# Performance work log

Measured on AMD Instinct MI355X. Metric: run time of the kernel, lower is better.

Reference implementation:

```python
import jax, jax.numpy as jnp
import numpy as np

N_NODES = 50000
N_EDGES = 1_000_000
N_HYPER = 1024
F_IN = 128
F_EDGE = 64


def setup_inputs() -> dict:
    key = jax.random.key(0)
    ks = jax.random.split(key, 20)
    s = 0.05
    return {
        "x": jax.random.normal(ks[0], (N_NODES, F_IN), jnp.float32),
        "edge_index": jax.random.randint(ks[1], (2, N_EDGES), 0, N_NODES, dtype=jnp.int64),
        "edge_weight": jax.random.uniform(ks[2], (N_EDGES,), jnp.float32),
        "edge_features": jax.random.normal(ks[3], (N_HYPER, F_EDGE), jnp.float32),
        "adj_e": jax.random.uniform(ks[4], (N_HYPER, N_HYPER), jnp.float32) / N_HYPER,
        "T": jax.random.uniform(ks[5], (N_NODES, N_HYPER), jnp.float32) / N_HYPER,
        # HypergraphConvLayer 1: 128 -> 64
        "W1": jax.random.normal(ks[6], (F_IN, 64), jnp.float32) * s,
        "b1": jnp.zeros((64,), jnp.float32),
        # HypergraphConvLayer 2: 64 -> 32
        "W2": jax.random.normal(ks[7], (64, 32), jnp.float32) * s,
        "b2": jnp.zeros((32,), jnp.float32),
        # GraphConvolution (CensNet-style): node 32->32, edge 64->32
        "Wn": jax.random.normal(ks[8], (32, 32), jnp.float32) * s,
        "We": jax.random.normal(ks[9], (F_EDGE, 32), jnp.float32) * s,
        "bg": jnp.zeros((32,), jnp.float32),
        # class_classifier: Linear(32,32) -> ReLU -> Linear(32,2) -> Softmax
        "Wc1": jax.random.normal(ks[10], (32, 32), jnp.float32) * s,
        "bc1": jnp.zeros((32,), jnp.float32),
        "Wc2": jax.random.normal(ks[11], (32, 2), jnp.float32) * s,
        "bc2": jnp.zeros((2,), jnp.float32),
    }


def _hconv(h, W, b, src, dst, edge_weight, num_nodes):
    # linear projection then edge-weighted scatter-add: out[dst] += w * h[src]
    h = h @ W + b
    msg = h[src] * edge_weight[:, None]          # [E, d]
    return jax.ops.segment_sum(msg, dst, num_segments=num_nodes)


def reference(x, edge_index, edge_weight, edge_features, adj_e, T,
              W1, b1, W2, b2, Wn, We, bg, Wc1, bc1, Wc2, bc2):
    n = x.shape[0]
    src, dst = edge_index[0], edge_index[1]

    h = jax.nn.relu(_hconv(x, W1, b1, src, dst, edge_weight, n))   # [N,64]
    h = jax.nn.relu(_hconv(h, W2, b2, src, dst, edge_weight, n))   # [N,32]

    # aggregate_node_features: node_features[dst] += h[src]; / num_edges
    num_edges = edge_index.shape[1]
    node_features = jax.ops.segment_sum(h[src], dst, num_segments=n) / num_edges

    # edge_conv: node linear + incidence-weighted hyperedge convolution
    edge_h = adj_e @ (edge_features @ We)                           # [NE,32]
    shared = jax.nn.relu(node_features @ Wn + T @ edge_h + bg)      # [N,32]

    # class_classifier
    c = jax.nn.relu(shared @ Wc1 + bc1)
    logits = c @ Wc2 + bc2
    return jax.nn.softmax(logits, axis=1)                           # [N,2]
```

## Files before the change

kernel.cpp:

```cpp
#include <hip/hip_runtime.h>
#include <hip/hip_bf16.h>

#define RPB 256

template<int COLS, int K>
__global__ __launch_bounds__(256) void gemm_k(
    const float* __restrict__ X, const float* __restrict__ W,
    const float* __restrict__ bias, float* __restrict__ out,
    int nrows, float scale, int relu_in)
{
    constexpr int CPT = COLS / 8;
    constexpr int KT  = 32;
    constexpr int NKT = K / KT;

    __shared__ float sx[RPB * 36];
    __shared__ float sWT[COLS * 33];

    const int tid = threadIdx.x;
    const int cg  = tid & 7;
    const int rg  = tid >> 3;
    const int r0  = blockIdx.x * RPB;

    float acc[8][CPT];
    #pragma unroll
    for (int r = 0; r < 8; ++r)
        #pragma unroll
        for (int c = 0; c < CPT; ++c) acc[r][c] = 0.f;

    for (int kt = 0; kt < NKT; ++kt) {
        #pragma unroll
        for (int j = 0; j < 8; ++j) {
            int i  = tid + j * 256;
            int r  = i >> 3;
            int k4 = i & 7;
            int gr = r0 + r; if (gr >= nrows) gr = nrows - 1;
            float4 v = *(const float4*)&X[(size_t)gr * K + kt * KT + k4 * 4];
            if (relu_in) {
                v.x = fmaxf(v.x, 0.f); v.y = fmaxf(v.y, 0.f);
                v.z = fmaxf(v.z, 0.f); v.w = fmaxf(v.w, 0.f);
            }
            if (scale != 1.f) { v.x *= scale; v.y *= scale; v.z *= scale; v.w *= scale; }
            *(float4*)&sx[r * 36 + k4 * 4] = v;
        }
        for (int i = tid; i < COLS * KT; i += 256) {
            int kl = i / COLS, c = i % COLS;
            sWT[c * 33 + kl] = W[(size_t)(kt * KT + kl) * COLS + c];
        }
        __syncthreads();

        #pragma unroll
        for (int k4 = 0; k4 < 8; ++k4) {
            float4 a[8];
            #pragma unroll
            for (int r = 0; r < 8; ++r)
                a[r] = *(const float4*)&sx[(r * 32 + rg) * 36 + k4 * 4];
            #pragma unroll
            for (int cc = 0; cc < CPT; ++cc) {
                int c = cg * CPT + cc;
                float w0 = sWT[c * 33 + k4 * 4 + 0];
                float w1 = sWT[c * 33 + k4 * 4 + 1];
                float w2 = sWT[c * 33 + k4 * 4 + 2];
                float w3 = sWT[c * 33 + k4 * 4 + 3];
                #pragma unroll
                for (int r = 0; r < 8; ++r)
                    acc[r][cc] += a[r].x * w0 + a[r].y * w1 + a[r].z * w2 + a[r].w * w3;
            }
        }
        __syncthreads();
    }

    #pragma unroll
    for (int r = 0; r < 8; ++r) {
        int row = r0 + r * 32 + rg;
        if (row < nrows) {
            #pragma unroll
            for (int cc4 = 0; cc4 < CPT / 4; ++cc4) {
                int c = cg * CPT + cc4 * 4;
                float4 o;
                o.x = acc[r][cc4 * 4 + 0] + (bias ? bias[c + 0] : 0.f);
                o.y = acc[r][cc4 * 4 + 1] + (bias ? bias[c + 1] : 0.f);
                o.z = acc[r][cc4 * 4 + 2] + (bias ? bias[c + 2] : 0.f);
                o.w = acc[r][cc4 * 4 + 3] + (bias ? bias[c + 3] : 0.f);
                *(float4*)&out[(size_t)row * COLS + c] = o;
            }
        }
    }
}

__global__ __launch_bounds__(256, 4) void tgemm2_k(
    const float* __restrict__ T, const float* __restrict__ eh,
    float* __restrict__ par, int nrows)
{
    __shared__ float seh[256 * 32];
    const int tid = threadIdx.x;
    const int ks  = blockIdx.y * 256;

    #pragma unroll
    for (int j = 0; j < 8; ++j) {
        int i = tid + j * 256;
        *(float4*)&seh[i * 4] = *(const float4*)&eh[(size_t)ks * 32 + (size_t)i * 4];
    }
    __syncthreads();

    int row = blockIdx.x * 256 + tid;
    int r   = row < nrows ? row : nrows - 1;
    const float* Tp = T + (size_t)r * 1024 + ks;

    float acc[32];
    #pragma unroll
    for (int c = 0; c < 32; ++c) acc[c] = 0.f;

    float4 t[8];
    #pragma unroll
    for (int q = 0; q < 8; ++q) t[q] = *(const float4*)&Tp[q * 4];

    for (int kc = 0; kc < 8; ++kc) {
        float4 tn[8];
        if (kc < 7) {
            #pragma unroll
            for (int q = 0; q < 8; ++q)
                tn[q] = *(const float4*)&Tp[(kc + 1) * 32 + q * 4];
        }
        #pragma unroll
        for (int q = 0; q < 8; ++q) {
            #pragma unroll
            for (int j = 0; j < 4; ++j) {
                float a = (j == 0) ? t[q].x : (j == 1) ? t[q].y : (j == 2) ? t[q].z : t[q].w;
                int k = kc * 32 + q * 4 + j;
                #pragma unroll
                for (int c4 = 0; c4 < 8; ++c4) {
                    float4 w = *(const float4*)&seh[k * 32 + c4 * 4];
                    acc[c4 * 4 + 0] += a * w.x;
                    acc[c4 * 4 + 1] += a * w.y;
                    acc[c4 * 4 + 2] += a * w.z;
                    acc[c4 * 4 + 3] += a * w.w;
                }
            }
        }
        #pragma unroll
        for (int q = 0; q < 8; ++q) t[q] = tn[q];
    }

    if (row < nrows) {
        float* p = par + (size_t)blockIdx.y * nrows * 32 + (size_t)row * 32;
        #pragma unroll
        for (int c4 = 0; c4 < 8; ++c4)
            *(float4*)&p[c4 * 4] = make_float4(acc[c4 * 4 + 0], acc[c4 * 4 + 1],
                                               acc[c4 * 4 + 2], acc[c4 * 4 + 3]);
    }
}

__global__ __launch_bounds__(256) void classify_k(
    const float* __restrict__ par, const float* __restrict__ nfw,
    const float* __restrict__ bg, const float* __restrict__ Wc1,
    const float* __restrict__ bc1, const float* __restrict__ Wc2,
    const float* __restrict__ bc2, float* __restrict__ out, int nrows)
{
    __shared__ float sWc1T[1024];
    __shared__ float sWc2[64];
    __shared__ float sb[66];

    int tid = threadIdx.x;
    for (int i = tid; i < 1024; i += 256)
        sWc1T[(i & 31) * 32 + (i >> 5)] = Wc1[i];
    if (tid < 64) sWc2[tid] = Wc2[tid];
    if (tid < 32)      sb[tid] = bc1[tid];
    else if (tid < 64) sb[tid] = bg[tid - 32];
    else if (tid < 66) sb[tid] = bc2[tid - 64];
    __syncthreads();

    int row = blockIdx.x * 256 + tid;
    if (row >= nrows) return;

    size_t stride = (size_t)nrows * 32;
    float4 sh4[8];
    #pragma unroll
    for (int i4 = 0; i4 < 8; ++i4) {
        const float* base = par + (size_t)row * 32 + i4 * 4;
        float4 v0 = *(const float4*)(base);
        float4 v1 = *(const float4*)(base + stride);
        float4 v2 = *(const float4*)(base + 2 * stride);
        float4 v3 = *(const float4*)(base + 3 * stride);
        float4 nf = *(const float4*)&nfw[(size_t)row * 32 + i4 * 4];
        float4 o;
        o.x = fmaxf(v0.x + v1.x + v2.x + v3.x + nf.x + sb[32 + i4 * 4 + 0], 0.f);
        o.y = fmaxf(v0.y + v1.y + v2.y + v3.y + nf.y + sb[32 + i4 * 4 + 1], 0.f);
        o.z = fmaxf(v0.z + v1.z + v2.z + v3.z + nf.z + sb[32 + i4 * 4 + 2], 0.f);
        o.w = fmaxf(v0.w + v1.w + v2.w + v3.w + nf.w + sb[32 + i4 * 4 + 3], 0.f);
        sh4[i4] = o;
    }

    float l0 = sb[64], l1 = sb[65];
    #pragma unroll
    for (int jj = 0; jj < 32; ++jj) {
        float s = sb[jj];
        #pragma unroll
        for (int i4 = 0; i4 < 8; ++i4) {
            float4 w4 = *(const float4*)&sWc1T[jj * 32 + i4 * 4];
            s += sh4[i4].x * w4.x + sh4[i4].y * w4.y
               + sh4[i4].z * w4.z + sh4[i4].w * w4.w;
        }
        s = fmaxf(s, 0.f);
        l0 += s * sWc2[jj * 2 + 0];
        l1 += s * sWc2[jj * 2 + 1];
    }
    float p0 = 1.f / (1.f + expf(l1 - l0));
    float p1 = 1.f / (1.f + expf(l0 - l1));
    *(float2*)&out[(size_t)row * 2] = make_float2(p0, p1);
}

__global__ void hist_k(const int* __restrict__ dst, int* __restrict__ deg, int E)
{
    int e = blockIdx.x * 256 + threadIdx.x;
    if (e < E) atomicAdd(&deg[dst[e]], 1);
}

__global__ void scan1_k(const int* __restrict__ deg, int* __restrict__ bsum, int N)
{
    __shared__ int s[256];
    int t = threadIdx.x, i = blockIdx.x * 256 + t;
    s[t] = (i < N) ? deg[i] : 0;
    __syncthreads();
    for (int off = 128; off > 0; off >>= 1) {
        if (t < off) s[t] += s[t + off];
        __syncthreads();
    }
    if (t == 0) bsum[blockIdx.x] = s[0];
}

__global__ void scan2_k(const int* __restrict__ bsum, int* __restrict__ boff,
                        int NB, int* __restrict__ rsN)
{
    __shared__ int s[256];
    int t = threadIdx.x;
    int v = (t < NB) ? bsum[t] : 0;
    s[t] = v;
    __syncthreads();
    for (int off = 1; off < 256; off <<= 1) {
        int u = (t >= off) ? s[t - off] : 0;
        __syncthreads();
        s[t] += u;
        __syncthreads();
    }
    if (t < NB) boff[t] = s[t] - v;
    if (t == NB - 1) *rsN = s[t];
}

__global__ void scan3_k(const int* __restrict__ deg, const int* __restrict__ boff,
                        int* __restrict__ rs, int* __restrict__ cur, int N)
{
    __shared__ int s[256];
    int t = threadIdx.x, i = blockIdx.x * 256 + t;
    int v = (i < N) ? deg[i] : 0;
    s[t] = v;
    __syncthreads();
    for (int off = 1; off < 256; off <<= 1) {
        int u = (t >= off) ? s[t - off] : 0;
        __syncthreads();
        s[t] += u;
        __syncthreads();
    }
    if (i < N) {
        int ex = boff[blockIdx.x] + s[t] - v;
        rs[i] = ex;
        cur[i] = ex;
    }
}

__global__ void fill_k(const int* __restrict__ src, const int* __restrict__ dst,
                       const float* __restrict__ ew, int* __restrict__ cur,
                       int* __restrict__ esrc, float* __restrict__ ews, int E)
{
    int e = blockIdx.x * 256 + threadIdx.x;
    if (e < E) {
        int pos = atomicAdd(&cur[dst[e]], 1);
        esrc[pos] = src[e];
        ews[pos]  = ew[e];
    }
}

__global__ __launch_bounds__(256) void gather64_k(
    const float* __restrict__ hp, const int* __restrict__ esrc,
    const float* __restrict__ ews, const int* __restrict__ rs,
    float* __restrict__ outv, int N)
{
    int lane = threadIdx.x & 63;
    int sub  = lane >> 4;
    int ch   = lane & 15;
    int wid  = (blockIdx.x * blockDim.x + threadIdx.x) >> 6;
    int nw   = (gridDim.x * blockDim.x) >> 6;
    for (int n = wid; n < N; n += nw) {
        int j0 = rs[n], j1 = rs[n + 1];
        float4 acc = make_float4(0.f, 0.f, 0.f, 0.f);
        for (int j = j0; j < j1; j += 8) {
            int ja = j + sub, jb = j + 4 + sub;
            bool va = ja < j1, vb = jb < j1;
            int ia = va ? ja : j0, ib = vb ? jb : j0;
            int sa = esrc[ia], sb2 = esrc[ib];
            float wa = va ? ews[ia] : 0.f;
            float wb = vb ? ews[ib] : 0.f;
            float4 v1 = *(const float4*)&hp[(size_t)sa * 64 + ch * 4];
            float4 v2 = *(const float4*)&hp[(size_t)sb2 * 64 + ch * 4];
            acc.x += v1.x * wa + v2.x * wb;
            acc.y += v1.y * wa + v2.y * wb;
            acc.z += v1.z * wa + v2.z * wb;
            acc.w += v1.w * wa + v2.w * wb;
        }
        acc.x += __shfl_xor(acc.x, 16); acc.y += __shfl_xor(acc.y, 16);
        acc.z += __shfl_xor(acc.z, 16); acc.w += __shfl_xor(acc.w, 16);
        acc.x += __shfl_xor(acc.x, 32); acc.y += __shfl_xor(acc.y, 32);
        acc.z += __shfl_xor(acc.z, 32); acc.w += __shfl_xor(acc.w, 32);
        if (lane < 16)
            *(float4*)&outv[(size_t)n * 64 + ch * 4] = acc;
    }
}

template<bool WEIGHTED, bool RELU>
__global__ __launch_bounds__(256) void gather32_k(
    const float* __restrict__ hp, const int* __restrict__ esrc,
    const float* __restrict__ ews, const int* __restrict__ rs,
    float* __restrict__ outv, int N)
{
    int lane = threadIdx.x & 63;
    int sub  = lane >> 3;
    int ch   = lane & 7;
    int wid  = (blockIdx.x * blockDim.x + threadIdx.x) >> 6;
    int nw   = (gridDim.x * blockDim.x) >> 6;
    for (int n = wid; n < N; n += nw) {
        int j0 = rs[n], j1 = rs[n + 1];
        float4 acc = make_float4(0.f, 0.f, 0.f, 0.f);
        for (int j = j0; j < j1; j += 16) {
            int ja = j + sub, jb = j + 8 + sub;
            bool va = ja < j1, vb = jb < j1;
            int ia = va ? ja : j0, ib = vb ? jb : j0;
            int sa = esrc[ia], sb2 = esrc[ib];
            float wa = WEIGHTED ? ews[ia] : 1.f;
            float wb = WEIGHTED ? ews[ib] : 1.f;
            if (!va) wa = 0.f;
            if (!vb) wb = 0.f;
            float4 v1 = *(const float4*)&hp[(size_t)sa * 32 + ch * 4];
            float4 v2 = *(const float4*)&hp[(size_t)sb2 * 32 + ch * 4];
            if (RELU) {
                v1.x = fmaxf(v1.x, 0.f); v1.y = fmaxf(v1.y, 0.f);
                v1.z = fmaxf(v1.z, 0.f); v1.w = fmaxf(v1.w, 0.f);
                v2.x = fmaxf(v2.x, 0.f); v2.y = fmaxf(v2.y, 0.f);
                v2.z = fmaxf(v2.z, 0.f); v2.w = fmaxf(v2.w, 0.f);
            }
            acc.x += v1.x * wa + v2.x * wb;
            acc.y += v1.y * wa + v2.y * wb;
            acc.z += v1.z * wa + v2.z * wb;
            acc.w += v1.w * wa + v2.w * wb;
        }
        acc.x += __shfl_xor(acc.x, 8);  acc.y += __shfl_xor(acc.y, 8);
        acc.z += __shfl_xor(acc.z, 8);  acc.w += __shfl_xor(acc.w, 8);
        acc.x += __shfl_xor(acc.x, 16); acc.y += __shfl_xor(acc.y, 16);
        acc.z += __shfl_xor(acc.z, 16); acc.w += __shfl_xor(acc.w, 16);
        acc.x += __shfl_xor(acc.x, 32); acc.y += __shfl_xor(acc.y, 32);
        acc.z += __shfl_xor(acc.z, 32); acc.w += __shfl_xor(acc.w, 32);
        if (lane < 8)
            *(float4*)&outv[(size_t)n * 32 + ch * 4] = acc;
    }
}

__global__ void efwe_k(const float* __restrict__ ef, const float* __restrict__ We,
                       float* __restrict__ tmp)
{
    int idx = blockIdx.x * 256 + threadIdx.x;
    int row = idx >> 5, c = idx & 31;
    float s = 0.f;
    #pragma unroll
    for (int k = 0; k < 64; ++k)
        s += ef[row * 64 + k] * We[k * 32 + c];
    tmp[row * 32 + c] = s;
}

__global__ void adjmm_k(const float* __restrict__ adj, const float* __restrict__ tmp,
                        float* __restrict__ edge_h)
{
    int kq     = blockIdx.x & 3;
    int rowblk = blockIdx.x >> 2;
    int r = rowblk * 8 + (threadIdx.x >> 5);
    int c = threadIdx.x & 31;
    float s = 0.f;
    int k0 = kq * 256;
    #pragma unroll 8
    for (int k = k0; k < k0 + 256; ++k)
        s += adj[r * 1024 + k] * tmp[k * 32 + c];
    atomicAdd(&edge_h[r * 32 + c], s);
}

extern "C" void kernel_launch(void* const* d_in, const int* in_sizes, int n_in,
                              void* d_out, int out_size, void* d_ws, size_t ws_size,
                              hipStream_t stream)
{
    const float* x   = (const float*)d_in[0];
    const int*   ei  = (const int*)  d_in[1];
    const float* ew  = (const float*)d_in[2];
    const float* ef  = (const float*)d_in[3];
    const float* adj = (const float*)d_in[4];
    const float* T   = (const float*)d_in[5];
    const float* W1  = (const float*)d_in[6];
    const float* b1  = (const float*)d_in[7];
    const float* W2  = (const float*)d_in[8];
    const float* b2  = (const float*)d_in[9];
    const float* Wn  = (const float*)d_in[10];
    const float* We  = (const float*)d_in[11];
    const float* bg  = (const float*)d_in[12];
    const float* Wc1 = (const float*)d_in[13];
    const float* bc1 = (const float*)d_in[14];
    const float* Wc2 = (const float*)d_in[15];
    const float* bc2 = (const float*)d_in[16];
    float* out = (float*)d_out;

    const int N = in_sizes[0] / 128;
    const int E = in_sizes[1] / 2;
    const int* srcIdx = ei;
    const int* dstIdx = ei + E;

    float* ws = (float*)d_ws;
    size_t o = 0;
    float* h1acc  = ws + o; o += (size_t)N * 64;
    float* h2acc  = ws + o; o += (size_t)N * 32;
    float* nfacc  = ws + o; o += (size_t)N * 32;
    float* edge_h = ws + o; o += 1024 * 32;
    float* tmp    = ws + o; o += 1024 * 32;
    float* nfw    = ws + o; o += (size_t)N * 32;
    float* par    = ws + o; o += (size_t)N * 128;
    float* h1p    = par;
    float* h2p    = par + (size_t)N * 64;
    int*   esrc   = (int*)(ws + o);   o += E;
    float* ews    = ws + o;           o += E;
    int*   deg    = (int*)(ws + o);   o += N;
    int*   rs     = (int*)(ws + o);   o += N + 1;
    int*   cur    = (int*)(ws + o);   o += N + 1;
    int*   bsum   = (int*)(ws + o);   o += 256;
    int*   boff   = (int*)(ws + o);   o += 256;

    const int NB = (N + 255) / 256;

    (void)hipMemsetAsync(deg, 0, (size_t)N * sizeof(int), stream);
    (void)hipMemsetAsync(edge_h, 0, 1024 * 32 * sizeof(float), stream);

    gemm_k<64, 128><<<NB, 256, 0, stream>>>(x, W1, b1, h1p, N, 1.f, 0);

    hist_k<<<(E + 255) / 256, 256, 0, stream>>>(dstIdx, deg, E);
    scan1_k<<<NB, 256, 0, stream>>>(deg, bsum, N);
    scan2_k<<<1, 256, 0, stream>>>(bsum, boff, NB, rs + N);
    scan3_k<<<NB, 256, 0, stream>>>(deg, boff, rs, cur, N);
    fill_k<<<(E + 255) / 256, 256, 0, stream>>>(srcIdx, dstIdx, ew, cur, esrc, ews, E);

    gather64_k<<<1024, 256, 0, stream>>>(h1p, esrc, ews, rs, h1acc, N);

    gemm_k<32, 64><<<NB, 256, 0, stream>>>(h1acc, W2, b2, h2p, N, 1.f, 1);

    gather32_k<true, false><<<1024, 256, 0, stream>>>(h2p, esrc, ews, rs, h2acc, N);

    gather32_k<false, true><<<1024, 256, 0, stream>>>(h2acc, esrc, ews, rs, nfacc, N);

    efwe_k<<<128, 256, 0, stream>>>(ef, We, tmp);
    adjmm_k<<<512, 256, 0, stream>>>(adj, tmp, edge_h);

    gemm_k<32, 32><<<NB, 256, 0, stream>>>(nfacc, Wn, nullptr, nfw, N, 1.f / (float)E, 0);

    tgemm2_k<<<dim3(NB, 4), 256, 0, stream>>>(T, edge_h, par, N);

    classify_k<<<NB, 256, 0, stream>>>(par, nfw, bg, Wc1, bc1, Wc2, bc2, out, N);
}
```

Baseline: 745.6 us.

## Fuse T-GEMM with classifier, simplify GEMMs, pack edge src/weight pairs

Replaces the tiled shared-memory GEMM with a one-row-per-thread kernel that reads weights directly from global memory (relying on cache broadcast). Fuses the T@edge_h product, node-feature add, ReLU and the classifier MLP plus softmax into one kernel, which removes the split-K partial buffer and the separate classify pass. Packs the CSR source index and edge weight into an int2 so each gather does one load per edge. The trade-off is lower parallelism in the T GEMM, since it drops from four K-split blocks per row tile to one, and weight reads go to global or cache instead of LDS.

```diff
diff --git a/kernel.cpp b/kernel.cpp
--- a/kernel.cpp
+++ b/kernel.cpp
@@ -1,135 +1,44 @@
 #include <hip/hip_runtime.h>
 #include <hip/hip_bf16.h>
 
-#define RPB 256
-
-template<int COLS, int K>
-__global__ __launch_bounds__(256) void gemm_k(
+template<int COLS, int K, bool RELU_IN>
+__global__ __launch_bounds__(256) void gemms_k(
     const float* __restrict__ X, const float* __restrict__ W,
     const float* __restrict__ bias, float* __restrict__ out,
-    int nrows, float scale, int relu_in)
-{
-    constexpr int CPT = COLS / 8;
-    constexpr int KT  = 32;
-    constexpr int NKT = K / KT;
-
-    __shared__ float sx[RPB * 36];
-    __shared__ float sWT[COLS * 33];
-
-    const int tid = threadIdx.x;
-    const int cg  = tid & 7;
-    const int rg  = tid >> 3;
-    const int r0  = blockIdx.x * RPB;
-
-    float acc[8][CPT];
-    #pragma unroll
-    for (int r = 0; r < 8; ++r)
-        #pragma unroll
-        for (int c = 0; c < CPT; ++c) acc[r][c] = 0.f;
-
-    for (int kt = 0; kt < NKT; ++kt) {
-        #pragma unroll
-        for (int j = 0; j < 8; ++j) {
-            int i  = tid + j * 256;
-            int r  = i >> 3;
-            int k4 = i & 7;
-            int gr = r0 + r; if (gr >= nrows) gr = nrows - 1;
-            float4 v = *(const float4*)&X[(size_t)gr * K + kt * KT + k4 * 4];
-            if (relu_in) {
-                v.x = fmaxf(v.x, 0.f); v.y = fmaxf(v.y, 0.f);
-                v.z = fmaxf(v.z, 0.f); v.w = fmaxf(v.w, 0.f);
-            }
-            if (scale != 1.f) { v.x *= scale; v.y *= scale; v.z *= scale; v.w *= scale; }
-            *(float4*)&sx[r * 36 + k4 * 4] = v;
-        }
-        for (int i = tid; i < COLS * KT; i += 256) {
-            int kl = i / COLS, c = i % COLS;
-            sWT[c * 33 + kl] = W[(size_t)(kt * KT + kl) * COLS + c];
-        }
-        __syncthreads();
-
-        #pragma unroll
-        for (int k4 = 0; k4 < 8; ++k4) {
-            float4 a[8];
-            #pragma unroll
-            for (int r = 0; r < 8; ++r)
-                a[r] = *(const float4*)&sx[(r * 32 + rg) * 36 + k4 * 4];
-            #pragma unroll
-            for (int cc = 0; cc < CPT; ++cc) {
-                int c = cg * CPT + cc;
-                float w0 = sWT[c * 33 + k4 * 4 + 0];
-                float w1 = sWT[c * 33 + k4 * 4 + 1];
-                float w2 = sWT[c * 33 + k4 * 4 + 2];
-                float w3 = sWT[c * 33 + k4 * 4 + 3];
-                #pragma unroll
-                for (int r = 0; r < 8; ++r)
-                    acc[r][cc] += a[r].x * w0 + a[r].y * w1 + a[r].z * w2 + a[r].w * w3;
-            }
-        }
-        __syncthreads();
-    }
-
-    #pragma unroll
-    for (int r = 0; r < 8; ++r) {
-        int row = r0 + r * 32 + rg;
-        if (row < nrows) {
-            #pragma unroll
-            for (int cc4 = 0; cc4 < CPT / 4; ++cc4) {
-                int c = cg * CPT + cc4 * 4;
-                float4 o;
-                o.x = acc[r][cc4 * 4 + 0] + (bias ? bias[c + 0] : 0.f);
-                o.y = acc[r][cc4 * 4 + 1] + (bias ? bias[c + 1] : 0.f);
-                o.z = acc[r][cc4 * 4 + 2] + (bias ? bias[c + 2] : 0.f);
-                o.w = acc[r][cc4 * 4 + 3] + (bias ? bias[c + 3] : 0.f);
-                *(float4*)&out[(size_t)row * COLS + c] = o;
-            }
-        }
-    }
-}
-
-__global__ __launch_bounds__(256, 4) void tgemm2_k(
-    const float* __restrict__ T, const float* __restrict__ eh,
-    float* __restrict__ par, int nrows)
-{
-    __shared__ float seh[256 * 32];
-    const int tid = threadIdx.x;
-    const int ks  = blockIdx.y * 256;
-
-    #pragma unroll
-    for (int j = 0; j < 8; ++j) {
-        int i = tid + j * 256;
-        *(float4*)&seh[i * 4] = *(const float4*)&eh[(size_t)ks * 32 + (size_t)i * 4];
-    }
-    __syncthreads();
-
-    int row = blockIdx.x * 256 + tid;
+    int nrows, float scale)
+{
+    constexpr int NC = K / 32;
+    int row = blockIdx.x * 256 + threadIdx.x;
     int r   = row < nrows ? row : nrows - 1;
-    const float* Tp = T + (size_t)r * 1024 + ks;
-
-    float acc[32];
-    #pragma unroll
-    for (int c = 0; c < 32; ++c) acc[c] = 0.f;
+    const float* Xp = X + (size_t)r * K;
+
+    float acc[COLS];
+    #pragma unroll
+    for (int c = 0; c < COLS; ++c) acc[c] = 0.f;
 
     float4 t[8];
     #pragma unroll
-    for (int q = 0; q < 8; ++q) t[q] = *(const float4*)&Tp[q * 4];
-
-    for (int kc = 0; kc < 8; ++kc) {
+    for (int q = 0; q < 8; ++q) t[q] = *(const float4*)&Xp[q * 4];
+
+    #pragma unroll 1
+    for (int kc = 0; kc < NC; ++kc) {
         float4 tn[8];
-        if (kc < 7) {
+        if (kc < NC - 1) {
             #pragma unroll
             for (int q = 0; q < 8; ++q)
-                tn[q] = *(const float4*)&Tp[(kc + 1) * 32 + q * 4];
+                tn[q] = *(const float4*)&Xp[(kc + 1) * 32 + q * 4];
         }
         #pragma unroll
         for (int q = 0; q < 8; ++q) {
             #pragma unroll
             for (int j = 0; j < 4; ++j) {
-                float a = (j == 0) ? t[q].x : (j == 1) ? t[q].y : (j == 2) ? t[q].z : t[q].w;
+                float a = (j == 0) ? t[q].x : (j == 1) ? t[q].y
+                        : (j == 2) ? t[q].z : t[q].w;
+                if (RELU_IN) a = fmaxf(a, 0.f);
                 int k = kc * 32 + q * 4 + j;
                 #pragma unroll
-                for (int c4 = 0; c4 < 8; ++c4) {
-                    float4 w = *(const float4*)&seh[k * 32 + c4 * 4];
+                for (int c4 = 0; c4 < COLS / 4; ++c4) {
+                    float4 w = *(const float4*)&W[(size_t)k * COLS + c4 * 4];
                     acc[c4 * 4 + 0] += a * w.x;
                     acc[c4 * 4 + 1] += a * w.y;
                     acc[c4 * 4 + 2] += a * w.z;
@@ -142,71 +51,92 @@
     }
 
     if (row < nrows) {
-        float* p = par + (size_t)blockIdx.y * nrows * 32 + (size_t)row * 32;
-        #pragma unroll
-        for (int c4 = 0; c4 < 8; ++c4)
-            *(float4*)&p[c4 * 4] = make_float4(acc[c4 * 4 + 0], acc[c4 * 4 + 1],
-                                               acc[c4 * 4 + 2], acc[c4 * 4 + 3]);
-    }
-}
-
-__global__ __launch_bounds__(256) void classify_k(
-    const float* __restrict__ par, const float* __restrict__ nfw,
-    const float* __restrict__ bg, const float* __restrict__ Wc1,
-    const float* __restrict__ bc1, const float* __restrict__ Wc2,
-    const float* __restrict__ bc2, float* __restrict__ out, int nrows)
-{
-    __shared__ float sWc1T[1024];
-    __shared__ float sWc2[64];
-    __shared__ float sb[66];
-
-    int tid = threadIdx.x;
-    for (int i = tid; i < 1024; i += 256)
-        sWc1T[(i & 31) * 32 + (i >> 5)] = Wc1[i];
-    if (tid < 64) sWc2[tid] = Wc2[tid];
-    if (tid < 32)      sb[tid] = bc1[tid];
-    else if (tid < 64) sb[tid] = bg[tid - 32];
-    else if (tid < 66) sb[tid] = bc2[tid - 64];
-    __syncthreads();
-
-    int row = blockIdx.x * 256 + tid;
-    if (row >= nrows) return;
-
-    size_t stride = (size_t)nrows * 32;
-    float4 sh4[8];
-    #pragma unroll
-    for (int i4 = 0; i4 < 8; ++i4) {
-        const float* base = par + (size_t)row * 32 + i4 * 4;
-        float4 v0 = *(const float4*)(base);
-        float4 v1 = *(const float4*)(base + stride);
-        float4 v2 = *(const float4*)(base + 2 * stride);
-        float4 v3 = *(const float4*)(base + 3 * stride);
-        float4 nf = *(const float4*)&nfw[(size_t)row * 32 + i4 * 4];
-        float4 o;
-        o.x = fmaxf(v0.x + v1.x + v2.x + v3.x + nf.x + sb[32 + i4 * 4 + 0], 0.f);
-        o.y = fmaxf(v0.y + v1.y + v2.y + v3.y + nf.y + sb[32 + i4 * 4 + 1], 0.f);
-        o.z = fmaxf(v0.z + v1.z + v2.z + v3.z + nf.z + sb[32 + i4 * 4 + 2], 0.f);
-        o.w = fmaxf(v0.w + v1.w + v2.w + v3.w + nf.w + sb[32 + i4 * 4 + 3], 0.f);
-        sh4[i4] = o;
-    }
-
-    float l0 = sb[64], l1 = sb[65];
-    #pragma unroll
-    for (int jj = 0; jj < 32; ++jj) {
-        float s = sb[jj];
-        #pragma unroll
-        for (int i4 = 0; i4 < 8; ++i4) {
-            float4 w4 = *(const float4*)&sWc1T[jj * 32 + i4 * 4];
-            s += sh4[i4].x * w4.x + sh4[i4].y * w4.y
-               + sh4[i4].z * w4.z + sh4[i4].w * w4.w;
-        }
+        #pragma unroll
+        for (int c4 = 0; c4 < COLS / 4; ++c4) {
+            float4 o;
+            o.x = acc[c4 * 4 + 0] * scale + (bias ? bias[c4 * 4 + 0] : 0.f);
+            o.y = acc[c4 * 4 + 1] * scale + (bias ? bias[c4 * 4 + 1] : 0.f);
+            o.z = acc[c4 * 4 + 2] * scale + (bias ? bias[c4 * 4 + 2] : 0.f);
+            o.w = acc[c4 * 4 + 3] * scale + (bias ? bias[c4 * 4 + 3] : 0.f);
+            *(float4*)&out[(size_t)row * COLS + c4 * 4] = o;
+        }
+    }
+}
+
+__global__ __launch_bounds__(256) void tfused_k(
+    const float* __restrict__ T, const float* __restrict__ eh,
+    const float* __restrict__ nfw, const float* __restrict__ bg,
+    const float* __restrict__ Wc1, const float* __restrict__ bc1,
+    const float* __restrict__ Wc2, const float* __restrict__ bc2,
+    float* __restrict__ out, int nrows)
+{
+    int row = blockIdx.x * 256 + threadIdx.x;
+    int r   = row < nrows ? row : nrows - 1;
+    const float* Tp = T + (size_t)r * 1024;
+
+    float acc[32];
+    #pragma unroll
+    for (int c = 0; c < 32; ++c) acc[c] = 0.f;
+
+    float4 t[8];
+    #pragma unroll
+    for (int q = 0; q < 8; ++q) t[q] = *(const float4*)&Tp[q * 4];
+
+    #pragma unroll 1
+    for (int kc = 0; kc < 32; ++kc) {
+        float4 tn[8];
+        if (kc < 31) {
+            #pragma unroll
+            for (int q = 0; q < 8; ++q)
+                tn[q] = *(const float4*)&Tp[(kc + 1) * 32 + q * 4];
+        }
+        #pragma unroll
+        for (int q = 0; q < 8; ++q) {
+            #pragma unroll
+            for (int j = 0; j < 4; ++j) {
+                float a = (j == 0) ? t[q].x : (j == 1) ? t[q].y
+                        : (j == 2) ? t[q].z : t[q].w;
+                int k = kc * 32 + q * 4 + j;
+                #pragma unroll
+                for (int c4 = 0; c4 < 8; ++c4) {
+                    float4 w = *(const float4*)&eh[(size_t)k * 32 + c4 * 4];
+                    acc[c4 * 4 + 0] += a * w.x;
+                    acc[c4 * 4 + 1] += a * w.y;
+                    acc[c4 * 4 + 2] += a * w.z;
+                    acc[c4 * 4 + 3] += a * w.w;
+                }
+            }
+        }
+        #pragma unroll
+        for (int q = 0; q < 8; ++q) t[q] = tn[q];
+    }
+
+    #pragma unroll
+    for (int c4 = 0; c4 < 8; ++c4) {
+        float4 nf = *(const float4*)&nfw[(size_t)r * 32 + c4 * 4];
+        acc[c4 * 4 + 0] = fmaxf(acc[c4 * 4 + 0] + nf.x + bg[c4 * 4 + 0], 0.f);
+        acc[c4 * 4 + 1] = fmaxf(acc[c4 * 4 + 1] + nf.y + bg[c4 * 4 + 1], 0.f);
+        acc[c4 * 4 + 2] = fmaxf(acc[c4 * 4 + 2] + nf.z + bg[c4 * 4 + 2], 0.f);
+        acc[c4 * 4 + 3] = fmaxf(acc[c4 * 4 + 3] + nf.w + bg[c4 * 4 + 3], 0.f);
+    }
+
+    float l0 = bc2[0], l1 = bc2[1];
+    #pragma unroll
+    for (int j = 0; j < 32; ++j) {
+        float s = bc1[j];
+        #pragma unroll
+        for (int i = 0; i < 32; ++i)
+            s += acc[i] * Wc1[i * 32 + j];
         s = fmaxf(s, 0.f);
-        l0 += s * sWc2[jj * 2 + 0];
-        l1 += s * sWc2[jj * 2 + 1];
-    }
-    float p0 = 1.f / (1.f + expf(l1 - l0));
-    float p1 = 1.f / (1.f + expf(l0 - l1));
-    *(float2*)&out[(size_t)row * 2] = make_float2(p0, p1);
+        l0 += s * Wc2[j * 2 + 0];
+        l1 += s * Wc2[j * 2 + 1];
+    }
+
+    if (row < nrows) {
+        float p0 = 1.f / (1.f + __expf(l1 - l0));
+        float p1 = 1.f / (1.f + __expf(l0 - l1));
+        *(float2*)&out[(size_t)row * 2] = make_float2(p0, p1);
+    }
 }
 
 __global__ void hist_k(const int* __restrict__ dst, int* __restrict__ deg, int E)
@@ -269,20 +199,18 @@
 
 __global__ void fill_k(const int* __restrict__ src, const int* __restrict__ dst,
                        const float* __restrict__ ew, int* __restrict__ cur,
-                       int* __restrict__ esrc, float* __restrict__ ews, int E)
+                       int2* __restrict__ epk, int E)
 {
     int e = blockIdx.x * 256 + threadIdx.x;
     if (e < E) {
         int pos = atomicAdd(&cur[dst[e]], 1);
-        esrc[pos] = src[e];
-        ews[pos]  = ew[e];
+        epk[pos] = make_int2(src[e], __float_as_int(ew[e]));
     }
 }
 
 __global__ __launch_bounds__(256) void gather64_k(
-    const float* __restrict__ hp, const int* __restrict__ esrc,
-    const float* __restrict__ ews, const int* __restrict__ rs,
-    float* __restrict__ outv, int N)
+    const float* __restrict__ hp, const int2* __restrict__ epk,
+    const int* __restrict__ rs, float* __restrict__ outv, int N)
 {
     int lane = threadIdx.x & 63;
     int sub  = lane >> 4;
@@ -295,12 +223,12 @@
         for (int j = j0; j < j1; j += 8) {
             int ja = j + sub, jb = j + 4 + sub;
             bool va = ja < j1, vb = jb < j1;
-            int ia = va ? ja : j0, ib = vb ? jb : j0;
-            int sa = esrc[ia], sb2 = esrc[ib];
-            float wa = va ? ews[ia] : 0.f;
-            float wb = vb ? ews[ib] : 0.f;
-            float4 v1 = *(const float4*)&hp[(size_t)sa * 64 + ch * 4];
-            float4 v2 = *(const float4*)&hp[(size_t)sb2 * 64 + ch * 4];
+            int2 ea = epk[va ? ja : j0];
+            int2 eb = epk[vb ? jb : j0];
+            float wa = va ? __int_as_float(ea.y) : 0.f;
+            float wb = vb ? __int_as_float(eb.y) : 0.f;
+            float4 v1 = *(const float4*)&hp[(size_t)ea.x * 64 + ch * 4];
+            float4 v2 = *(const float4*)&hp[(size_t)eb.x * 64 + ch * 4];
             acc.x += v1.x * wa + v2.x * wb;
             acc.y += v1.y * wa + v2.y * wb;
             acc.z += v1.z * wa + v2.z * wb;
@@ -317,9 +245,8 @@
 
 template<bool WEIGHTED, bool RELU>
 __global__ __launch_bounds__(256) void gather32_k(
-    const float* __restrict__ hp, const int* __restrict__ esrc,
-    const float* __restrict__ ews, const int* __restrict__ rs,
-    float* __restrict__ outv, int N)
+    const float* __restrict__ hp, const int2* __restrict__ epk,
+    const int* __restrict__ rs, float* __restrict__ outv, int N)
 {
     int lane = threadIdx.x & 63;
     int sub  = lane >> 3;
@@ -332,14 +259,14 @@
         for (int j = j0; j < j1; j += 16) {
             int ja = j + sub, jb = j + 8 + sub;
             bool va = ja < j1, vb = jb < j1;
-            int ia = va ? ja : j0, ib = vb ? jb : j0;
-            int sa = esrc[ia], sb2 = esrc[ib];
-            float wa = WEIGHTED ? ews[ia] : 1.f;
-            float wb = WEIGHTED ? ews[ib] : 1.f;
+            int2 ea = epk[va ? ja : j0];
+            int2 eb = epk[vb ? jb : j0];
+            float wa = WEIGHTED ? __int_as_float(ea.y) : 1.f;
+            float wb = WEIGHTED ? __int_as_float(eb.y) : 1.f;
             if (!va) wa = 0.f;
             if (!vb) wb = 0.f;
-            float4 v1 = *(const float4*)&hp[(size_t)sa * 32 + ch * 4];
-            float4 v2 = *(const float4*)&hp[(size_t)sb2 * 32 + ch * 4];
+            float4 v1 = *(const float4*)&hp[(size_t)ea.x * 32 + ch * 4];
+            float4 v2 = *(const float4*)&hp[(size_t)eb.x * 32 + ch * 4];
             if (RELU) {
                 v1.x = fmaxf(v1.x, 0.f); v1.y = fmaxf(v1.y, 0.f);
                 v1.z = fmaxf(v1.z, 0.f); v1.w = fmaxf(v1.w, 0.f);
@@ -425,11 +352,9 @@
     float* edge_h = ws + o; o += 1024 * 32;
     float* tmp    = ws + o; o += 1024 * 32;
     float* nfw    = ws + o; o += (size_t)N * 32;
-    float* par    = ws + o; o += (size_t)N * 128;
-    float* h1p    = par;
-    float* h2p    = par + (size_t)N * 64;
-    int*   esrc   = (int*)(ws + o);   o += E;
-    float* ews    = ws + o;           o += E;
+    float* h1p    = ws + o; o += (size_t)N * 64;
+    float* h2p    = ws + o; o += (size_t)N * 32;
+    int2*  epk    = (int2*)(ws + o);  o += (size_t)E * 2;
     int*   deg    = (int*)(ws + o);   o += N;
     int*   rs     = (int*)(ws + o);   o += N + 1;
     int*   cur    = (int*)(ws + o);   o += N + 1;
@@ -441,28 +366,26 @@
     (void)hipMemsetAsync(deg, 0, (size_t)N * sizeof(int), stream);
     (void)hipMemsetAsync(edge_h, 0, 1024 * 32 * sizeof(float), stream);
 
-    gemm_k<64, 128><<<NB, 256, 0, stream>>>(x, W1, b1, h1p, N, 1.f, 0);
+    gemms_k<64, 128, false><<<NB, 256, 0, stream>>>(x, W1, b1, h1p, N, 1.f);
 
     hist_k<<<(E + 255) / 256, 256, 0, stream>>>(dstIdx, deg, E);
     scan1_k<<<NB, 256, 0, stream>>>(deg, bsum, N);
     scan2_k<<<1, 256, 0, stream>>>(bsum, boff, NB, rs + N);
     scan3_k<<<NB, 256, 0, stream>>>(deg, boff, rs, cur, N);
-    fill_k<<<(E + 255) / 256, 256, 0, stream>>>(srcIdx, dstIdx, ew, cur, esrc, ews, E);
-
-    gather64_k<<<1024, 256, 0, stream>>>(h1p, esrc, ews, rs, h1acc, N);
-
-    gemm_k<32, 64><<<NB, 256, 0, stream>>>(h1acc, W2, b2, h2p, N, 1.f, 1);
-
-    gather32_k<true, false><<<1024, 256, 0, stream>>>(h2p, esrc, ews, rs, h2acc, N);
-
-    gather32_k<false, true><<<1024, 256, 0, stream>>>(h2acc, esrc, ews, rs, nfacc, N);
+    fill_k<<<(E + 255) / 256, 256, 0, stream>>>(srcIdx, dstIdx, ew, cur, epk, E);
+
+    gather64_k<<<1024, 256, 0, stream>>>(h1p, epk, rs, h1acc, N);
+
+    gemms_k<32, 64, true><<<NB, 256, 0, stream>>>(h1acc, W2, b2, h2p, N, 1.f);
+
+    gather32_k<true, false><<<1024, 256, 0, stream>>>(h2p, epk, rs, h2acc, N);
+
+    gather32_k<false, true><<<1024, 256, 0, stream>>>(h2acc, epk, rs, nfacc, N);
 
     efwe_k<<<128, 256, 0, stream>>>(ef, We, tmp);
     adjmm_k<<<512, 256, 0, stream>>>(adj, tmp, edge_h);
 
-    gemm_k<32, 32><<<NB, 256, 0, stream>>>(nfacc, Wn, nullptr, nfw, N, 1.f / (float)E, 0);
-
-    tgemm2_k<<<dim3(NB, 4), 256, 0, stream>>>(T, edge_h, par, N);
-
-    classify_k<<<NB, 256, 0, stream>>>(par, nfw, bg, Wc1, bc1, Wc2, bc2, out, N);
-}
+    gemms_k<32, 32, false><<<NB, 256, 0, stream>>>(nfacc, Wn, nullptr, nfw, N, 1.f / (float)E);
+
+    tfused_k<<<NB, 256, 0, stream>>>(T, edge_h, nfw, bg, Wc1, bc1, Wc2, bc2, out, N);
+}
```

After: 1.348 ms. 1.81x slower.
